# Performance work log

Measured on AMD Instinct MI355X. Metric: run time of the kernel, lower is better.

The kernel has to match this reference:

```python
import jax, jax.numpy as jnp
import numpy as np

B, CIN, COUT, R = 8, 256, 256, 128  # H = W = R (required by the module's permute-then-conv structure)


def _init_linear(key, out_c, in_c):
    # mimic torch Conv2d(kernel=1) default init: uniform(-1/sqrt(fan_in), 1/sqrt(fan_in))
    k1, k2 = jax.random.split(key)
    bound = 1.0 / np.sqrt(in_c)
    W = jax.random.uniform(k1, (out_c, in_c), jnp.float32, -bound, bound)
    b = jax.random.uniform(k2, (out_c,), jnp.float32, -bound, bound)
    return W, b


def setup_inputs() -> dict:
    key = jax.random.key(0)
    keys = jax.random.split(key, 9)
    x = jax.random.normal(keys[0], (B, CIN, R, R), jnp.float32)
    Wr, br = _init_linear(keys[1], R, CIN)          # resize conv
    Wqw, bqw = _init_linear(keys[2], R, R)          # width-attn q (mixes over H axis, H==R)
    Wkw, bkw = _init_linear(keys[3], R, R)
    Wvw, bvw = _init_linear(keys[4], R, R)
    Wqh, bqh = _init_linear(keys[5], R, R)          # height-attn q (mixes over W axis, W==R)
    Wkh, bkh = _init_linear(keys[6], R, R)
    Wvh, bvh = _init_linear(keys[7], R, R)
    Wo, bo = _init_linear(keys[8], COUT, R)         # restore conv
    return dict(x=x, Wr=Wr, br=br, Wqw=Wqw, bqw=bqw, Wkw=Wkw, bkw=bkw, Wvw=Wvw, bvw=bvw,
                Wqh=Wqh, bqh=bqh, Wkh=Wkh, bkh=bkh, Wvh=Wvh, bvh=bvh, Wo=Wo, bo=bo)


def _csaa_forward(x, Wr, br, Wqw, bqw, Wkw, bkw, Wvw, bvw, Wqh, bqh, Wkh, bkh, Wvh, bvh, Wo, bo):
    # resize 1x1 conv: [B,CIN,H,W] -> [B,R,H,W]
    resized = jnp.einsum('oc,bchw->bohw', Wr, x) + br[None, :, None, None]

    # --- width-branch AxialAttention (height_dim=False) ---
    # permute(0,2,1,3): [B,R,H,W] -> [B,H,R,W]; 1x1 conv now mixes over the H axis (H==R)
    xp = jnp.transpose(resized, (0, 2, 1, 3))                      # [B,H,R,W]
    q = jnp.einsum('oh,bhrw->borw', Wqw, xp) + bqw[None, :, None, None]
    k = jnp.einsum('oh,bhrw->borw', Wkw, xp) + bkw[None, :, None, None]
    v = jnp.einsum('oh,bhrw->borw', Wvw, xp) + bvw[None, :, None, None]
    attn = jax.nn.softmax(jnp.einsum('borw,bouw->boru', q, k), axis=-1)  # [B,O,R,R]
    out = jnp.einsum('boru,bouw->borw', attn, v)                   # [B,O,R,W]
    w_attn = jnp.transpose(out, (0, 2, 1, 3))                      # [B,R,O,W] == [B,R,H,W]

    # --- height-branch AxialAttention (height_dim=True) ---
    # permute(0,3,1,2): [B,R,H,W] -> [B,W,R,H]; 1x1 conv mixes over the W axis (W==R)
    xp = jnp.transpose(w_attn, (0, 3, 1, 2))                       # [B,W,R,H]
    q = jnp.einsum('ow,bwrh->borh', Wqh, xp) + bqh[None, :, None, None]
    k = jnp.einsum('ow,bwrh->borh', Wkh, xp) + bkh[None, :, None, None]
    v = jnp.einsum('ow,bwrh->borh', Wvh, xp) + bvh[None, :, None, None]
    attn = jax.nn.softmax(jnp.einsum('borh,bouh->boru', q, k), axis=-1)  # [B,O,R,R]
    out = jnp.einsum('boru,bouh->borh', attn, v)                   # [B,O,R,H]
    h_attn = jnp.transpose(out, (0, 2, 3, 1))                      # [B,R,H,O] == [B,R,H,W]

    # restore 1x1 conv: [B,R,H,W] -> [B,COUT,H,W]
    return jnp.einsum('oc,bchw->bohw', Wo, h_attn) + bo[None, :, None, None]


def reference(x, Wr, br, Wqw, bqw, Wkw, bkw, Wvw, bvw, Wqh, bqh, Wkh, bkh, Wvh, bvh, Wo, bo):
    return _csaa_forward(x, Wr, br, Wqw, bqw, Wkw, bkw, Wvw, bvw,
                         Wqh, bqh, Wkh, bkh, Wvh, bvh, Wo, bo)
```

## Files before the change

kernel.cpp:

```cpp
#include <hip/hip_runtime.h>
#include <hip/hip_bf16.h>


typedef __attribute__((ext_vector_type(8))) short bf16x8;
typedef __attribute__((ext_vector_type(4))) float f32x4;

__device__ __forceinline__ short f2b(float f) {
    __hip_bfloat16 h = __float2bfloat16(f);
    short s; __builtin_memcpy(&s, &h, 2);
    return s;
}

__device__ __forceinline__ int swx(int row) { return (row ^ (row >> 3)) & 7; }
__device__ __forceinline__ int swzb(int row, int blk) {
    return (row << 7) + ((blk ^ swx(row)) << 3);
}

__device__ __forceinline__ void gload16(const void* g, void* l) {
    __builtin_amdgcn_global_load_lds(
        (const __attribute__((address_space(1))) void*)g,
        (__attribute__((address_space(3))) void*)l, 16, 0, 0);
}

__device__ __forceinline__ void mfma128(const short* __restrict__ SA,
                                        const short* __restrict__ SB,
                                        f32x4 (&acc)[4][4], int lane,
                                        int wr64, int wc64) {
    #pragma unroll
    for (int kk = 0; kk < 4; kk++) {
        const int kb = kk * 4 + (lane >> 4);
        bf16x8 a[4], b[4];
        #pragma unroll
        for (int mi = 0; mi < 4; mi++)
            a[mi] = *(const bf16x8*)&SA[swzb(wr64 + mi * 16 + (lane & 15), kb)];
        #pragma unroll
        for (int ni = 0; ni < 4; ni++)
            b[ni] = *(const bf16x8*)&SB[swzb(wc64 + ni * 16 + (lane & 15), kb)];
        #pragma unroll
        for (int mi = 0; mi < 4; mi++)
            #pragma unroll
            for (int ni = 0; ni < 4; ni++)
                acc[mi][ni] = __builtin_amdgcn_mfma_f32_16x16x32_bf16(
                    a[mi], b[ni], acc[mi][ni], 0, 0, 0);
    }
}

__device__ __forceinline__ void mfma64x128(const short* __restrict__ SA,
                                           const short* __restrict__ SB,
                                           f32x4 (&acc)[2][4], int lane,
                                           int wr32, int wc64) {
    #pragma unroll
    for (int kk = 0; kk < 4; kk++) {
        const int kb = kk * 4 + (lane >> 4);
        bf16x8 a[2], b[4];
        #pragma unroll
        for (int mi = 0; mi < 2; mi++)
            a[mi] = *(const bf16x8*)&SA[swzb(wr32 + mi * 16 + (lane & 15), kb)];
        #pragma unroll
        for (int ni = 0; ni < 4; ni++)
            b[ni] = *(const bf16x8*)&SB[swzb(wc64 + ni * 16 + (lane & 15), kb)];
        #pragma unroll
        for (int mi = 0; mi < 2; mi++)
            #pragma unroll
            for (int ni = 0; ni < 4; ni++)
                acc[mi][ni] = __builtin_amdgcn_mfma_f32_16x16x32_bf16(
                    a[mi], b[ni], acc[mi][ni], 0, 0, 0);
    }
}

__device__ __forceinline__ void stage_nf_bf16(const short* __restrict__ Bb,
                                              long long b_r, int k0,
                                              short* __restrict__ Bs, int t) {
    const int n8 = t & 15, kb = t >> 4;
    bf16x8 rk[8];
    #pragma unroll
    for (int i = 0; i < 8; i++)
        rk[i] = *(const bf16x8*)(Bb + (long long)(k0 + kb * 8 + i) * b_r + n8 * 8);
    #pragma unroll
    for (int j = 0; j < 8; j++) {
        bf16x8 col;
        #pragma unroll
        for (int i = 0; i < 8; i++) col[i] = rk[i][j];
        *(bf16x8*)&Bs[swzb(n8 * 8 + j, kb)] = col;
    }
}

__device__ __forceinline__ void stage_nf_f32(const float* __restrict__ Bb,
                                             long long b_r, int k0,
                                             short* __restrict__ Bs, int t) {
    const int n8 = t & 15, kb = t >> 4;
    bf16x8 rk[8];
    #pragma unroll
    for (int i = 0; i < 8; i++) {
        const float* s = Bb + (long long)(k0 + kb * 8 + i) * b_r + n8 * 8;
        float4 v0 = *(const float4*)s, v1 = *(const float4*)(s + 4);
        rk[i][0] = f2b(v0.x); rk[i][1] = f2b(v0.y);
        rk[i][2] = f2b(v0.z); rk[i][3] = f2b(v0.w);
        rk[i][4] = f2b(v1.x); rk[i][5] = f2b(v1.y);
        rk[i][6] = f2b(v1.z); rk[i][7] = f2b(v1.w);
    }
    #pragma unroll
    for (int j = 0; j < 8; j++) {
        bf16x8 col;
        #pragma unroll
        for (int i = 0; i < 8; i++) col[i] = rk[i][j];
        *(bf16x8*)&Bs[swzb(n8 * 8 + j, kb)] = col;
    }
}

__global__ __launch_bounds__(256)
void wprep(const float* __restrict__ Wr, const float* __restrict__ Wqw,
           const float* __restrict__ Wkw, const float* __restrict__ Wvw,
           const float* __restrict__ Wqh, const float* __restrict__ Wkh,
           const float* __restrict__ Wvh, const float* __restrict__ Wo,
           short* __restrict__ dst) {
    const int id = blockIdx.y;
    const float* W; int M, K, off;
    switch (id) {
        case 0: W = Wr;  M = 128; K = 256; off = 0;      break;
        case 1: W = Wqw; M = 128; K = 128; off = 32768;  break;
        case 2: W = Wkw; M = 128; K = 128; off = 49152;  break;
        case 3: W = Wvw; M = 128; K = 128; off = 65536;  break;
        case 4: W = Wqh; M = 128; K = 128; off = 81920;  break;
        case 5: W = Wkh; M = 128; K = 128; off = 98304;  break;
        case 6: W = Wvh; M = 128; K = 128; off = 114688; break;
        default: W = Wo; M = 256; K = 128; off = 131072; break;
    }
    int g = blockIdx.x * 256 + threadIdx.x;
    if (g >= (M * K) >> 3) return;
    int gpr = K >> 3;
    int row = g / gpr;
    int blk = g - row * gpr;
    int ks = blk >> 4, bi = blk & 15;
    int my = row >> 7, r = row & 127;
    int nks = K >> 7;
    const float* s = W + (long long)row * K + blk * 8;
    float4 v0 = *(const float4*)s, v1 = *(const float4*)(s + 4);
    bf16x8 ov;
    ov[0] = f2b(v0.x); ov[1] = f2b(v0.y); ov[2] = f2b(v0.z); ov[3] = f2b(v0.w);
    ov[4] = f2b(v1.x); ov[5] = f2b(v1.y); ov[6] = f2b(v1.z); ov[7] = f2b(v1.w);
    *(bf16x8*)(dst + off + (my * nks + ks) * 16384 + swzb(r, bi)) = ov;
}

__global__ __launch_bounds__(256)
void gemm_p1(const short* __restrict__ A0, const float* __restrict__ bias0,
             const float* __restrict__ Bsrc,
             long long b_z, long long b_x, long long b_r,
             short* __restrict__ C0,
             long long c_z, long long c_x, long long c_m) {
    __shared__ short As[16384];
    __shared__ short Bs[16384];
    const int t = threadIdx.x;
    const int lane = t & 63;
    const int wid = t >> 6;
    const int wr64 = (wid >> 1) * 64, wc64 = (wid & 1) * 64;
    const int bx = blockIdx.x, bz = blockIdx.z;

    f32x4 acc[4][4];
    #pragma unroll
    for (int mi = 0; mi < 4; mi++)
        #pragma unroll
        for (int ni = 0; ni < 4; ni++) acc[mi][ni] = (f32x4){0.f, 0.f, 0.f, 0.f};

    for (int ks = 0; ks < 2; ks++) {
        if (ks) __syncthreads();
        stage_nf_f32(Bsrc + bz * b_z + bx * b_x, b_r, ks * 128, Bs, t);
        const short* Ai = A0 + ks * 16384;
        #pragma unroll
        for (int i = 0; i < 8; i++) {
            int q = wid * 8 + i;
            gload16(Ai + q * 512 + lane * 8, &As[q * 512]);
        }
        __syncthreads();
        mfma128(As, Bs, acc, lane, wr64, wc64);
    }
    __syncthreads();

    #pragma unroll
    for (int mi = 0; mi < 4; mi++)
        #pragma unroll
        for (int r = 0; r < 4; r++) {
            int row = wr64 + mi * 16 + (lane >> 4) * 4 + r;
            float bb = bias0[row];
            #pragma unroll
            for (int ni = 0; ni < 4; ni++) {
                int col = wc64 + ni * 16 + (lane & 15);
                As[swzb(row, col >> 3) + (col & 7)] = f2b(acc[mi][ni][r] + bb);
            }
        }
    __syncthreads();
    short* Cg = C0 + bz * c_z + bx * c_x;
    #pragma unroll
    for (int i = 0; i < 8; i++) {
        int idx = t + i * 256;
        int row = idx >> 4, ch = idx & 15;
        *(bf16x8*)(Cg + (long long)row * c_m + ch * 8) =
            *(const bf16x8*)&As[swzb(row, ch)];
    }
}

template<int NW, int BMODE, bool F32OUT>
__global__ __launch_bounds__(256, 3)
void gemmw64(const short* __restrict__ A0, const short* __restrict__ A1,
             const short* __restrict__ A2,
             const float* __restrict__ bias0, const float* __restrict__ bias1,
             const float* __restrict__ bias2,
             const void* __restrict__ Bsrc, long long b_z, long long b_x,
             long long b_r,
             short* __restrict__ C0, short* __restrict__ C1,
             short* __restrict__ C2, float* __restrict__ Cf,
             long long c_z, long long c_x, long long c_m) {
    __shared__ short As[8192];
    __shared__ short Bs[16384];
    const int t = threadIdx.x;
    const int lane = t & 63;
    const int wid = t >> 6;
    const int wr32 = (wid >> 1) * 32, wc64 = (wid & 1) * 64;
    const int bx = blockIdx.x, my = blockIdx.y, bz = blockIdx.z;
    const int mbase = my * 64;

    if (BMODE == 0) {
        const short* Bb = (const short*)Bsrc + bz * b_z + bx * b_x;
        #pragma unroll
        for (int i = 0; i < 8; i++) {
            int q = wid * 8 + i;
            int row = q * 4 + (lane >> 4);
            gload16(Bb + (long long)row * b_r + (((lane & 15) ^ swx(row)) << 3),
                    &Bs[q * 512]);
        }
    } else {
        stage_nf_bf16((const short*)Bsrc + bz * b_z + bx * b_x, b_r, 0, Bs, t);
    }

    #pragma unroll
    for (int g = 0; g < NW; g++) {
        if (g) __syncthreads();
        const short* Ai = ((g == 0) ? A0 : (g == 1) ? A1 : A2) + my * 8192;
        #pragma unroll
        for (int i = 0; i < 4; i++) {
            int q = wid * 4 + i;
            gload16(Ai + q * 512 + lane * 8, &As[q * 512]);
        }
        __syncthreads();

        f32x4 acc[2][4];
        #pragma unroll
        for (int mi = 0; mi < 2; mi++)
            #pragma unroll
            for (int ni = 0; ni < 4; ni++)
                acc[mi][ni] = (f32x4){0.f, 0.f, 0.f, 0.f};
        mfma64x128(As, Bs, acc, lane, wr32, wc64);

        const float* bias = (g == 0) ? bias0 : (g == 1) ? bias1 : bias2;
        if (F32OUT) {
            float* Cb = Cf + bz * c_z + bx * c_x;
            #pragma unroll
            for (int mi = 0; mi < 2; mi++)
                #pragma unroll
                for (int r = 0; r < 4; r++) {
                    int row = mbase + wr32 + mi * 16 + (lane >> 4) * 4 + r;
                    float bb = bias[row];
                    float* cp = Cb + (long long)row * c_m + wc64 + (lane & 15);
                    #pragma unroll
                    for (int ni = 0; ni < 4; ni++)
                        cp[ni * 16] = acc[mi][ni][r] + bb;
                }
        } else {
            __syncthreads();
            #pragma unroll
            for (int mi = 0; mi < 2; mi++)
                #pragma unroll
                for (int r = 0; r < 4; r++) {
                    int row = wr32 + mi * 16 + (lane >> 4) * 4 + r;
                    float bb = bias[mbase + row];
                    #pragma unroll
                    for (int ni = 0; ni < 4; ni++) {
                        int col = wc64 + ni * 16 + (lane & 15);
                        As[swzb(row, col >> 3) + (col & 7)] =
                            f2b(acc[mi][ni][r] + bb);
                    }
                }
            __syncthreads();
            short* Cg = ((g == 0) ? C0 : (g == 1) ? C1 : C2)
                      + bz * c_z + bx * c_x;
            #pragma unroll
            for (int i = 0; i < 4; i++) {
                int idx = t + i * 256;
                int row = idx >> 4, ch = idx & 15;
                *(bf16x8*)(Cg + (long long)(mbase + row) * c_m + ch * 8) =
                    *(const bf16x8*)&As[swzb(row, ch)];
            }
        }
    }
}

template<bool TEPI>
__global__ __launch_bounds__(256)
void attnk(const short* __restrict__ Q, const short* __restrict__ Kp,
           const short* __restrict__ V, short* __restrict__ O) {
    __shared__ short SA[16384];
    __shared__ short SB[16384];
    __shared__ float pmax[2][128];
    __shared__ float psum[2][128];
    const int t = threadIdx.x;
    const int lane = t & 63;
    const int wid = t >> 6;
    const int wr64 = (wid >> 1) * 64, wc64 = (wid & 1) * 64, wch = wid & 1;
    const long long poff = (long long)blockIdx.z * 2097152LL
                         + (long long)blockIdx.x * 16384LL;
    const short* Qb = Q + poff;
    const short* Kb = Kp + poff;
    const short* Vb = V + poff;
    short* Ob = O + (long long)blockIdx.z * 2097152LL + (long long)blockIdx.x * 128LL;

    #pragma unroll
    for (int i = 0; i < 8; i++) {
        int q = wid * 8 + i;
        int row = q * 4 + (lane >> 4);
        int sw = (((lane & 15) ^ swx(row)) << 3);
        gload16(Qb + row * 128 + sw, &SA[q * 512]);
        gload16(Kb + row * 128 + sw, &SB[q * 512]);
    }
    __syncthreads();

    f32x4 acc[4][4];
    #pragma unroll
    for (int mi = 0; mi < 4; mi++)
        #pragma unroll
        for (int ni = 0; ni < 4; ni++) acc[mi][ni] = (f32x4){0.f, 0.f, 0.f, 0.f};
    mfma128(SA, SB, acc, lane, wr64, wc64);

    #pragma unroll
    for (int mi = 0; mi < 4; mi++)
        #pragma unroll
        for (int r = 0; r < 4; r++) {
            float mx = fmaxf(fmaxf(acc[mi][0][r], acc[mi][1][r]),
                             fmaxf(acc[mi][2][r], acc[mi][3][r]));
            #pragma unroll
            for (int d = 1; d < 16; d <<= 1) mx = fmaxf(mx, __shfl_xor(mx, d, 64));
            if ((lane & 15) == 0)
                pmax[wch][wr64 + mi * 16 + (lane >> 4) * 4 + r] = mx;
        }
    __syncthreads();

    const int n8 = t & 15, kb = t >> 4;
    bf16x8 vk[8];
    #pragma unroll
    for (int i = 0; i < 8; i++)
        vk[i] = *(const bf16x8*)(Vb + (kb * 8 + i) * 128 + n8 * 8);

    #pragma unroll
    for (int mi = 0; mi < 4; mi++)
        #pragma unroll
        for (int r = 0; r < 4; r++) {
            int row = wr64 + mi * 16 + (lane >> 4) * 4 + r;
            float M = fmaxf(pmax[0][row], pmax[1][row]);
            float p[4], s = 0.f;
            #pragma unroll
            for (int ni = 0; ni < 4; ni++) {
                p[ni] = __expf(acc[mi][ni][r] - M);
                s += p[ni];
            }
            #pragma unroll
            for (int d = 1; d < 16; d <<= 1) s += __shfl_xor(s, d, 64);
            if ((lane & 15) == 0) psum[wch][row] = s;
            #pragma unroll
            for (int ni = 0; ni < 4; ni++) {
                int col = wc64 + ni * 16 + (lane & 15);
                SA[swzb(row, col >> 3) + (col & 7)] = f2b(p[ni]);
            }
        }
    #pragma unroll
    for (int j = 0; j < 8; j++) {
        bf16x8 col;
        #pragma unroll
        for (int i = 0; i < 8; i++) col[i] = vk[i][j];
        *(bf16x8*)&SB[swzb(n8 * 8 + j, kb)] = col;
    }
    __syncthreads();

    f32x4 acc2[4][4];
    #pragma unroll
    for (int mi = 0; mi < 4; mi++)
        #pragma unroll
        for (int ni = 0; ni < 4; ni++) acc2[mi][ni] = (f32x4){0.f, 0.f, 0.f, 0.f};
    mfma128(SA, SB, acc2, lane, wr64, wc64);
    __syncthreads();

    #pragma unroll
    for (int mi = 0; mi < 4; mi++)
        #pragma unroll
        for (int r = 0; r < 4; r++) {
            int row = wr64 + mi * 16 + (lane >> 4) * 4 + r;
            float rinv = 1.f / (psum[0][row] + psum[1][row]);
            #pragma unroll
            for (int ni = 0; ni < 4; ni++) {
                int col = wc64 + ni * 16 + (lane & 15);
                short vv = f2b(acc2[mi][ni][r] * rinv);
                if (!TEPI) SB[swzb(row, col >> 3) + (col & 7)] = vv;
                else       SB[swzb(col, row >> 3) + (row & 7)] = vv;
            }
        }
    __syncthreads();
    #pragma unroll
    for (int i = 0; i < 8; i++) {
        int idx = t + i * 256;
        int row = idx >> 4, ch = idx & 15;
        *(bf16x8*)(Ob + (long long)row * 16384 + ch * 8) =
            *(const bf16x8*)&SB[swzb(row, ch)];
    }
}

extern "C" void kernel_launch(void* const* d_in, const int* in_sizes, int n_in,
                              void* d_out, int out_size, void* d_ws, size_t ws_size,
                              hipStream_t stream) {
    const float* x   = (const float*)d_in[0];
    const float* Wr  = (const float*)d_in[1];
    const float* br  = (const float*)d_in[2];
    const float* Wqw = (const float*)d_in[3];
    const float* bqw = (const float*)d_in[4];
    const float* Wkw = (const float*)d_in[5];
    const float* bkw = (const float*)d_in[6];
    const float* Wvw = (const float*)d_in[7];
    const float* bvw = (const float*)d_in[8];
    const float* Wqh = (const float*)d_in[9];
    const float* bqh = (const float*)d_in[10];
    const float* Wkh = (const float*)d_in[11];
    const float* bkh = (const float*)d_in[12];
    const float* Wvh = (const float*)d_in[13];
    const float* bvh = (const float*)d_in[14];
    const float* Wo  = (const float*)d_in[15];
    const float* bo  = (const float*)d_in[16];
    float* out = (float*)d_out;
    (void)in_sizes; (void)n_in; (void)out_size; (void)ws_size;

    const long long U = 16777216LL;
    short* wsp = (short*)d_ws;
    short* s0 = wsp;
    short* s1 = wsp + U;
    short* s2 = wsp + 2 * U;
    short* s3 = wsp + 3 * U;
    short* wb = wsp + 4 * U;
    short* wWr  = wb;
    short* wWqw = wb + 32768;
    short* wWkw = wb + 49152;
    short* wWvw = wb + 65536;
    short* wWqh = wb + 81920;
    short* wWkh = wb + 98304;
    short* wWvh = wb + 114688;
    short* wWo  = wb + 131072;

    dim3 blk(256);

    wprep<<<dim3(16, 8), blk, 0, stream>>>(Wr, Wqw, Wkw, Wvw, Wqh, Wkh, Wvh, Wo, wb);

    gemm_p1<<<dim3(128, 1, 8), blk, 0, stream>>>(
        wWr, br, x, 4194304LL, 128LL, 16384LL,
        s0, 2097152LL, 128LL, 16384LL);

    gemmw64<3, 1, false><<<dim3(128, 2, 8), blk, 0, stream>>>(
        wWqw, wWkw, wWvw, bqw, bkw, bvw,
        s0, 2097152LL, 16384LL, 128LL,
        s1, s2, s3, nullptr, 2097152LL, 128LL, 16384LL);

    attnk<false><<<dim3(128, 1, 8), blk, 0, stream>>>(s1, s2, s3, s0);

    gemmw64<3, 0, false><<<dim3(128, 2, 8), blk, 0, stream>>>(
        wWqh, wWkh, wWvh, bqh, bkh, bvh,
        s0, 2097152LL, 16384LL, 128LL,
        s1, s2, s3, nullptr, 2097152LL, 128LL, 16384LL);

    attnk<true><<<dim3(128, 1, 8), blk, 0, stream>>>(s1, s2, s3, s0);

    gemmw64<1, 0, true><<<dim3(128, 4, 8), blk, 0, stream>>>(
        wWo, nullptr, nullptr, bo, nullptr, nullptr,
        s0, 2097152LL, 16384LL, 128LL,
        nullptr, nullptr, nullptr, out, 4194304LL, 128LL, 16384LL);
}
```

Measured before the change: 235.3 us.

## Repartition MFMA warps by full rows to drop cross-warp softmax and barriers

Each wave now owns whole output rows (32x128 or 16x128 strips) instead of 64x64 quadrants. Softmax max and sum can then be reduced inside one wave with shuffles, with no shared pmax/psum arrays. Several __syncthreads are removed because each wave writes and reads back only its own rows in the epilogue. In the grouped QKV GEMM, the next weight tile is loaded after the store. The trade-off is more B-fragment LDS reads per wave and higher register pressure, plus possible LDS hazards where barriers were dropped.

```diff
diff --git a/kernel.cpp b/kernel.cpp
--- a/kernel.cpp
+++ b/kernel.cpp
@@ -22,49 +22,43 @@
         (__attribute__((address_space(3))) void*)l, 16, 0, 0);
 }
 
-__device__ __forceinline__ void mfma128(const short* __restrict__ SA,
-                                        const short* __restrict__ SB,
-                                        f32x4 (&acc)[4][4], int lane,
-                                        int wr64, int wc64) {
+__device__ __forceinline__ void mfma32x128(const short* __restrict__ SA,
+                                           const short* __restrict__ SB,
+                                           f32x4 (&acc)[2][8], int lane, int wr) {
     #pragma unroll
     for (int kk = 0; kk < 4; kk++) {
         const int kb = kk * 4 + (lane >> 4);
-        bf16x8 a[4], b[4];
-        #pragma unroll
-        for (int mi = 0; mi < 4; mi++)
-            a[mi] = *(const bf16x8*)&SA[swzb(wr64 + mi * 16 + (lane & 15), kb)];
-        #pragma unroll
-        for (int ni = 0; ni < 4; ni++)
-            b[ni] = *(const bf16x8*)&SB[swzb(wc64 + ni * 16 + (lane & 15), kb)];
-        #pragma unroll
-        for (int mi = 0; mi < 4; mi++)
-            #pragma unroll
-            for (int ni = 0; ni < 4; ni++)
+        bf16x8 a[2], b[8];
+        #pragma unroll
+        for (int mi = 0; mi < 2; mi++)
+            a[mi] = *(const bf16x8*)&SA[swzb(wr + mi * 16 + (lane & 15), kb)];
+        #pragma unroll
+        for (int ni = 0; ni < 8; ni++)
+            b[ni] = *(const bf16x8*)&SB[swzb(ni * 16 + (lane & 15), kb)];
+        #pragma unroll
+        for (int mi = 0; mi < 2; mi++)
+            #pragma unroll
+            for (int ni = 0; ni < 8; ni++)
                 acc[mi][ni] = __builtin_amdgcn_mfma_f32_16x16x32_bf16(
                     a[mi], b[ni], acc[mi][ni], 0, 0, 0);
     }
 }
 
-__device__ __forceinline__ void mfma64x128(const short* __restrict__ SA,
+__device__ __forceinline__ void mfma16x128(const short* __restrict__ SA,
                                            const short* __restrict__ SB,
-                                           f32x4 (&acc)[2][4], int lane,
-                                           int wr32, int wc64) {
+                                           f32x4 (&acc)[8], int lane, int wr16) {
     #pragma unroll
     for (int kk = 0; kk < 4; kk++) {
         const int kb = kk * 4 + (lane >> 4);
-        bf16x8 a[2], b[4];
-        #pragma unroll
-        for (int mi = 0; mi < 2; mi++)
-            a[mi] = *(const bf16x8*)&SA[swzb(wr32 + mi * 16 + (lane & 15), kb)];
-        #pragma unroll
-        for (int ni = 0; ni < 4; ni++)
-            b[ni] = *(const bf16x8*)&SB[swzb(wc64 + ni * 16 + (lane & 15), kb)];
-        #pragma unroll
-        for (int mi = 0; mi < 2; mi++)
-            #pragma unroll
-            for (int ni = 0; ni < 4; ni++)
-                acc[mi][ni] = __builtin_amdgcn_mfma_f32_16x16x32_bf16(
-                    a[mi], b[ni], acc[mi][ni], 0, 0, 0);
+        bf16x8 a = *(const bf16x8*)&SA[swzb(wr16 + (lane & 15), kb)];
+        bf16x8 b[8];
+        #pragma unroll
+        for (int ni = 0; ni < 8; ni++)
+            b[ni] = *(const bf16x8*)&SB[swzb(ni * 16 + (lane & 15), kb)];
+        #pragma unroll
+        for (int ni = 0; ni < 8; ni++)
+            acc[ni] = __builtin_amdgcn_mfma_f32_16x16x32_bf16(
+                a, b[ni], acc[ni], 0, 0, 0);
     }
 }
 
@@ -153,15 +147,16 @@
     const int t = threadIdx.x;
     const int lane = t & 63;
     const int wid = t >> 6;
-    const int wr64 = (wid >> 1) * 64, wc64 = (wid & 1) * 64;
+    const int wr = wid * 32;
     const int bx = blockIdx.x, bz = blockIdx.z;
 
-    f32x4 acc[4][4];
-    #pragma unroll
-    for (int mi = 0; mi < 4; mi++)
-        #pragma unroll
-        for (int ni = 0; ni < 4; ni++) acc[mi][ni] = (f32x4){0.f, 0.f, 0.f, 0.f};
-
+    f32x4 acc[2][8];
+    #pragma unroll
+    for (int mi = 0; mi < 2; mi++)
+        #pragma unroll
+        for (int ni = 0; ni < 8; ni++) acc[mi][ni] = (f32x4){0.f, 0.f, 0.f, 0.f};
+
+    #pragma unroll
     for (int ks = 0; ks < 2; ks++) {
         if (ks) __syncthreads();
         stage_nf_f32(Bsrc + bz * b_z + bx * b_x, b_r, ks * 128, Bs, t);
@@ -172,28 +167,26 @@
             gload16(Ai + q * 512 + lane * 8, &As[q * 512]);
         }
         __syncthreads();
-        mfma128(As, Bs, acc, lane, wr64, wc64);
-    }
-    __syncthreads();
-
-    #pragma unroll
-    for (int mi = 0; mi < 4; mi++)
+        mfma32x128(As, Bs, acc, lane, wr);
+    }
+
+    #pragma unroll
+    for (int mi = 0; mi < 2; mi++)
         #pragma unroll
         for (int r = 0; r < 4; r++) {
-            int row = wr64 + mi * 16 + (lane >> 4) * 4 + r;
+            int row = wr + mi * 16 + (lane >> 4) * 4 + r;
             float bb = bias0[row];
             #pragma unroll
-            for (int ni = 0; ni < 4; ni++) {
-                int col = wc64 + ni * 16 + (lane & 15);
+            for (int ni = 0; ni < 8; ni++) {
+                int col = ni * 16 + (lane & 15);
                 As[swzb(row, col >> 3) + (col & 7)] = f2b(acc[mi][ni][r] + bb);
             }
         }
-    __syncthreads();
     short* Cg = C0 + bz * c_z + bx * c_x;
     #pragma unroll
     for (int i = 0; i < 8; i++) {
-        int idx = t + i * 256;
-        int row = idx >> 4, ch = idx & 15;
+        int idx = lane + i * 64;
+        int row = wr + (idx >> 4), ch = idx & 15;
         *(bf16x8*)(Cg + (long long)row * c_m + ch * 8) =
             *(const bf16x8*)&As[swzb(row, ch)];
     }
@@ -215,7 +208,7 @@
     const int t = threadIdx.x;
     const int lane = t & 63;
     const int wid = t >> 6;
-    const int wr32 = (wid >> 1) * 32, wc64 = (wid & 1) * 64;
+    const int wr16 = wid * 16;
     const int bx = blockIdx.x, my = blockIdx.y, bz = blockIdx.z;
     const int mbase = my * 64;
 
@@ -231,65 +224,64 @@
     } else {
         stage_nf_bf16((const short*)Bsrc + bz * b_z + bx * b_x, b_r, 0, Bs, t);
     }
-
-    #pragma unroll
-    for (int g = 0; g < NW; g++) {
-        if (g) __syncthreads();
-        const short* Ai = ((g == 0) ? A0 : (g == 1) ? A1 : A2) + my * 8192;
+    {
+        const short* Ai = A0 + my * 8192;
         #pragma unroll
         for (int i = 0; i < 4; i++) {
             int q = wid * 4 + i;
             gload16(Ai + q * 512 + lane * 8, &As[q * 512]);
         }
-        __syncthreads();
-
-        f32x4 acc[2][4];
-        #pragma unroll
-        for (int mi = 0; mi < 2; mi++)
-            #pragma unroll
-            for (int ni = 0; ni < 4; ni++)
-                acc[mi][ni] = (f32x4){0.f, 0.f, 0.f, 0.f};
-        mfma64x128(As, Bs, acc, lane, wr32, wc64);
-
+    }
+    __syncthreads();
+
+    #pragma unroll
+    for (int g = 0; g < NW; g++) {
         const float* bias = (g == 0) ? bias0 : (g == 1) ? bias1 : bias2;
+        f32x4 acc[8];
+        #pragma unroll
+        for (int ni = 0; ni < 8; ni++) acc[ni] = (f32x4){0.f, 0.f, 0.f, 0.f};
+        mfma16x128(As, Bs, acc, lane, wr16);
+
         if (F32OUT) {
             float* Cb = Cf + bz * c_z + bx * c_x;
             #pragma unroll
-            for (int mi = 0; mi < 2; mi++)
+            for (int r = 0; r < 4; r++) {
+                int row = mbase + wr16 + (lane >> 4) * 4 + r;
+                float bb = bias[row];
+                float* cp = Cb + (long long)row * c_m + (lane & 15);
                 #pragma unroll
-                for (int r = 0; r < 4; r++) {
-                    int row = mbase + wr32 + mi * 16 + (lane >> 4) * 4 + r;
-                    float bb = bias[row];
-                    float* cp = Cb + (long long)row * c_m + wc64 + (lane & 15);
-                    #pragma unroll
-                    for (int ni = 0; ni < 4; ni++)
-                        cp[ni * 16] = acc[mi][ni][r] + bb;
+                for (int ni = 0; ni < 8; ni++)
+                    cp[ni * 16] = acc[ni][r] + bb;
+            }
+        } else {
+            #pragma unroll
+            for (int r = 0; r < 4; r++) {
+                int row = wr16 + (lane >> 4) * 4 + r;
+                float bb = bias[mbase + row];
+                #pragma unroll
+                for (int ni = 0; ni < 8; ni++) {
+                    int col = ni * 16 + (lane & 15);
+                    As[swzb(row, col >> 3) + (col & 7)] = f2b(acc[ni][r] + bb);
                 }
-        } else {
-            __syncthreads();
-            #pragma unroll
-            for (int mi = 0; mi < 2; mi++)
-                #pragma unroll
-                for (int r = 0; r < 4; r++) {
-                    int row = wr32 + mi * 16 + (lane >> 4) * 4 + r;
-                    float bb = bias[mbase + row];
-                    #pragma unroll
-                    for (int ni = 0; ni < 4; ni++) {
-                        int col = wc64 + ni * 16 + (lane & 15);
-                        As[swzb(row, col >> 3) + (col & 7)] =
-                            f2b(acc[mi][ni][r] + bb);
-                    }
-                }
-            __syncthreads();
+            }
             short* Cg = ((g == 0) ? C0 : (g == 1) ? C1 : C2)
                       + bz * c_z + bx * c_x;
             #pragma unroll
             for (int i = 0; i < 4; i++) {
-                int idx = t + i * 256;
-                int row = idx >> 4, ch = idx & 15;
+                int idx = lane + i * 64;
+                int row = wr16 + (idx >> 4), ch = idx & 15;
                 *(bf16x8*)(Cg + (long long)(mbase + row) * c_m + ch * 8) =
                     *(const bf16x8*)&As[swzb(row, ch)];
             }
+        }
+        if (g + 1 < NW) {
+            const short* Ai = ((g == 0) ? A1 : A2) + my * 8192;
+            #pragma unroll
+            for (int i = 0; i < 4; i++) {
+                int q = wid * 4 + i;
+                gload16(Ai + q * 512 + lane * 8, &As[q * 512]);
+            }
+            __syncthreads();
         }
     }
 }
@@ -300,12 +292,10 @@
            const short* __restrict__ V, short* __restrict__ O) {
     __shared__ short SA[16384];
     __shared__ short SB[16384];
-    __shared__ float pmax[2][128];
-    __shared__ float psum[2][128];
     const int t = threadIdx.x;
     const int lane = t & 63;
     const int wid = t >> 6;
-    const int wr64 = (wid >> 1) * 64, wc64 = (wid & 1) * 64, wch = wid & 1;
+    const int wr = wid * 32;
     const long long poff = (long long)blockIdx.z * 2097152LL
                          + (long long)blockIdx.x * 16384LL;
     const short* Qb = Q + poff;
@@ -321,55 +311,49 @@
         gload16(Qb + row * 128 + sw, &SA[q * 512]);
         gload16(Kb + row * 128 + sw, &SB[q * 512]);
     }
-    __syncthreads();
-
-    f32x4 acc[4][4];
-    #pragma unroll
-    for (int mi = 0; mi < 4; mi++)
-        #pragma unroll
-        for (int ni = 0; ni < 4; ni++) acc[mi][ni] = (f32x4){0.f, 0.f, 0.f, 0.f};
-    mfma128(SA, SB, acc, lane, wr64, wc64);
-
-    #pragma unroll
-    for (int mi = 0; mi < 4; mi++)
-        #pragma unroll
-        for (int r = 0; r < 4; r++) {
-            float mx = fmaxf(fmaxf(acc[mi][0][r], acc[mi][1][r]),
-                             fmaxf(acc[mi][2][r], acc[mi][3][r]));
-            #pragma unroll
-            for (int d = 1; d < 16; d <<= 1) mx = fmaxf(mx, __shfl_xor(mx, d, 64));
-            if ((lane & 15) == 0)
-                pmax[wch][wr64 + mi * 16 + (lane >> 4) * 4 + r] = mx;
-        }
-    __syncthreads();
-
     const int n8 = t & 15, kb = t >> 4;
     bf16x8 vk[8];
     #pragma unroll
     for (int i = 0; i < 8; i++)
         vk[i] = *(const bf16x8*)(Vb + (kb * 8 + i) * 128 + n8 * 8);
-
-    #pragma unroll
-    for (int mi = 0; mi < 4; mi++)
+    __syncthreads();
+
+    f32x4 acc[2][8];
+    #pragma unroll
+    for (int mi = 0; mi < 2; mi++)
+        #pragma unroll
+        for (int ni = 0; ni < 8; ni++) acc[mi][ni] = (f32x4){0.f, 0.f, 0.f, 0.f};
+    mfma32x128(SA, SB, acc, lane, wr);
+
+    float rs[2][4];
+    #pragma unroll
+    for (int mi = 0; mi < 2; mi++)
         #pragma unroll
         for (int r = 0; r < 4; r++) {
-            int row = wr64 + mi * 16 + (lane >> 4) * 4 + r;
-            float M = fmaxf(pmax[0][row], pmax[1][row]);
-            float p[4], s = 0.f;
-            #pragma unroll
-            for (int ni = 0; ni < 4; ni++) {
-                p[ni] = __expf(acc[mi][ni][r] - M);
+            float mx = acc[mi][0][r];
+            #pragma unroll
+            for (int ni = 1; ni < 8; ni++) mx = fmaxf(mx, acc[mi][ni][r]);
+            #pragma unroll
+            for (int d = 1; d < 16; d <<= 1) mx = fmaxf(mx, __shfl_xor(mx, d, 64));
+            float s = 0.f;
+            float p[8];
+            #pragma unroll
+            for (int ni = 0; ni < 8; ni++) {
+                p[ni] = __expf(acc[mi][ni][r] - mx);
                 s += p[ni];
             }
             #pragma unroll
             for (int d = 1; d < 16; d <<= 1) s += __shfl_xor(s, d, 64);
-            if ((lane & 15) == 0) psum[wch][row] = s;
-            #pragma unroll
-            for (int ni = 0; ni < 4; ni++) {
-                int col = wc64 + ni * 16 + (lane & 15);
+            rs[mi][r] = 1.f / s;
+            int row = wr + mi * 16 + (lane >> 4) * 4 + r;
+            #pragma unroll
+            for (int ni = 0; ni < 8; ni++) {
+                int col = ni * 16 + (lane & 15);
                 SA[swzb(row, col >> 3) + (col & 7)] = f2b(p[ni]);
             }
         }
+    __syncthreads();
+
     #pragma unroll
     for (int j = 0; j < 8; j++) {
         bf16x8 col;
@@ -379,35 +363,55 @@
     }
     __syncthreads();
 
-    f32x4 acc2[4][4];
-    #pragma unroll
-    for (int mi = 0; mi < 4; mi++)
-        #pragma unroll
-        for (int ni = 0; ni < 4; ni++) acc2[mi][ni] = (f32x4){0.f, 0.f, 0.f, 0.f};
-    mfma128(SA, SB, acc2, lane, wr64, wc64);
-    __syncthreads();
-
-    #pragma unroll
-    for (int mi = 0; mi < 4; mi++)
-        #pragma unroll
-        for (int r = 0; r < 4; r++) {
-            int row = wr64 + mi * 16 + (lane >> 4) * 4 + r;
-            float rinv = 1.f / (psum[0][row] + psum[1][row]);
-            #pragma unroll
-            for (int ni = 0; ni < 4; ni++) {
-                int col = wc64 + ni * 16 + (lane & 15);
-                short vv = f2b(acc2[mi][ni][r] * rinv);
-                if (!TEPI) SB[swzb(row, col >> 3) + (col & 7)] = vv;
-                else       SB[swzb(col, row >> 3) + (row & 7)] = vv;
-            }
-        }
-    __syncthreads();
-    #pragma unroll
-    for (int i = 0; i < 8; i++) {
-        int idx = t + i * 256;
-        int row = idx >> 4, ch = idx & 15;
-        *(bf16x8*)(Ob + (long long)row * 16384 + ch * 8) =
-            *(const bf16x8*)&SB[swzb(row, ch)];
+    f32x4 acc2[2][8];
+    #pragma unroll
+    for (int mi = 0; mi < 2; mi++)
+        #pragma unroll
+        for (int ni = 0; ni < 8; ni++) acc2[mi][ni] = (f32x4){0.f, 0.f, 0.f, 0.f};
+    mfma32x128(SA, SB, acc2, lane, wr);
+
+    if (!TEPI) {
+        #pragma unroll
+        for (int mi = 0; mi < 2; mi++)
+            #pragma unroll
+            for (int r = 0; r < 4; r++) {
+                int row = wr + mi * 16 + (lane >> 4) * 4 + r;
+                float rinv = rs[mi][r];
+                #pragma unroll
+                for (int ni = 0; ni < 8; ni++) {
+                    int col = ni * 16 + (lane & 15);
+                    SA[swzb(row, col >> 3) + (col & 7)] = f2b(acc2[mi][ni][r] * rinv);
+                }
+            }
+        #pragma unroll
+        for (int i = 0; i < 8; i++) {
+            int idx = lane + i * 64;
+            int row = wr + (idx >> 4), ch = idx & 15;
+            *(bf16x8*)(Ob + (long long)row * 16384 + ch * 8) =
+                *(const bf16x8*)&SA[swzb(row, ch)];
+        }
+    } else {
+        __syncthreads();
+        #pragma unroll
+        for (int mi = 0; mi < 2; mi++)
+            #pragma unroll
+            for (int r = 0; r < 4; r++) {
+                int row = wr + mi * 16 + (lane >> 4) * 4 + r;
+                float rinv = rs[mi][r];
+                #pragma unroll
+                for (int ni = 0; ni < 8; ni++) {
+                    int col = ni * 16 + (lane & 15);
+                    SB[swzb(col, row >> 3) + (row & 7)] = f2b(acc2[mi][ni][r] * rinv);
+                }
+            }
+        __syncthreads();
+        #pragma unroll
+        for (int i = 0; i < 8; i++) {
+            int idx = t + i * 256;
+            int row = idx >> 4, ch = idx & 15;
+            *(bf16x8*)(Ob + (long long)row * 16384 + ch * 8) =
+                *(const bf16x8*)&SB[swzb(row, ch)];
+        }
     }
 }
 
```

Result: faster. 216.7 us (-7.9%).
